# Optimization experiments

Measured on AMD Instinct MI355X. Metric: run time of the kernel, lower is better.

## Reference

```python
import jax, jax.numpy as jnp
import numpy as np

N = 50000      # nodes
E = 800000     # edges (avg degree 16)
D = 64         # emb_dim
L = 5          # num_layer
BN_EPS = 1e-5


def setup_inputs() -> dict:
    key = jax.random.key(0)
    ks = jax.random.split(key, 10)
    x = jax.random.randint(ks[0], (N,), 0, 1)                      # indices into 1-row embedding
    edge_index = jax.random.randint(ks[1], (2, E), 0, N)
    edge_attr = jax.random.normal(ks[2], (E, 7), dtype=jnp.float32)
    s = lambda k, shape: (jax.random.normal(k, shape, dtype=jnp.float32) * 0.05)
    node_emb = s(ks[3], (1, D))
    # per-layer GINConv params, stacked on a leading layer axis for lax.scan
    We = s(ks[4], (L, 7, D));   be = jnp.zeros((L, D), jnp.float32)      # edge_encoder
    eps = jnp.zeros((L,), jnp.float32)                                   # GIN eps
    W1 = s(ks[5], (L, D, 2 * D)); b1 = jnp.zeros((L, 2 * D), jnp.float32)  # mlp linear1
    g1 = jnp.ones((L, 2 * D), jnp.float32); bb1 = jnp.zeros((L, 2 * D), jnp.float32)  # mlp BN
    W2 = s(ks[6], (L, 2 * D, D)); b2 = jnp.zeros((L, D), jnp.float32)    # mlp linear2
    g2 = jnp.ones((L, D), jnp.float32); bb2 = jnp.zeros((L, D), jnp.float32)  # outer BN
    return dict(x=x, edge_index=edge_index, edge_attr=edge_attr, node_emb=node_emb,
                We=We, be=be, eps=eps, W1=W1, b1=b1, g1=g1, bb1=bb1,
                W2=W2, b2=b2, g2=g2, bb2=bb2)


def _bn(a, g, b):
    # BatchNorm1d in training mode: batch statistics over node axis, biased var
    m = a.mean(axis=0)
    v = jnp.var(a, axis=0)
    return (a - m) * jax.lax.rsqrt(v + BN_EPS) * g + b


def reference(x, edge_index, edge_attr, node_emb, We, be, eps,
              W1, b1, g1, bb1, W2, b2, g2, bb2):
    src, dst = edge_index[0], edge_index[1]
    h = node_emb[x]                                    # [N, D]
    relu_flags = jnp.arange(L) < (L - 1)               # ReLU on all but last layer

    def step(h, p):
        We_, be_, eps_, W1_, b1_, g1_, bb1_, W2_, b2_, g2_, bb2_, flag = p
        ee = edge_attr @ We_ + be_                     # [E, D] edge embeddings
        msg = jax.nn.relu(h[src] + ee)                 # gather + elementwise
        agg = jax.ops.segment_sum(msg, dst, num_segments=N)  # scatter-add
        z = (1.0 + eps_) * h + agg                     # GIN combine
        a = jax.nn.relu(_bn(z @ W1_ + b1_, g1_, bb1_)) # mlp: lin -> BN -> ReLU
        hb = _bn(a @ W2_ + b2_, g2_, bb2_)             # lin -> outer BN
        h_new = jnp.where(flag, jax.nn.relu(hb), hb)   # dropout omitted (eval)
        return h_new, None

    h, _ = jax.lax.scan(step, h, (We, be, eps, W1, b1, g1, bb1, W2, b2, g2, bb2, relu_flags))
    return h                                           # JK='last'
```

## Files before the change

kernel.cpp:

```cpp
#include <hip/hip_runtime.h>
#include <hip/hip_fp16.h>

#define NN 50000
#define EE 800000
#define NB 782
#define NBKT 196
#define CAP8 736

typedef _Float16 f16x8 __attribute__((ext_vector_type(8)));
typedef _Float16 f16x4 __attribute__((ext_vector_type(4)));
typedef _Float16 f16x2 __attribute__((ext_vector_type(2)));
typedef float f32x4 __attribute__((ext_vector_type(4)));

__device__ __forceinline__ unsigned h2u(__half2 h) {
    union { __half2 h; unsigned u; } c; c.h = h; return c.u;
}
__device__ __forceinline__ f16x2 u2h(unsigned u) {
    union { unsigned u; f16x2 h; } c; c.u = u; return c.h;
}

__global__ __launch_bounds__(256) void bin_kernel(
    const int* __restrict__ ei, const float* __restrict__ ea,
    int* __restrict__ bktcur, int4* __restrict__ srec,
    unsigned short* __restrict__ sdst)
{
    __shared__ int cnt[NBKT], base[NBKT];
    const int t = threadIdx.x;
    const int xid = blockIdx.x & 7;
    if (t < NBKT) cnt[t] = 0;
    __syncthreads();
    const int e0 = blockIdx.x << 10;
    int bkk[4], rk[4], loc[4];
#pragma unroll
    for (int j = 0; j < 4; ++j) {
        const int e = e0 + (j << 8) + t;
        if (e < EE) {
            const int d = ei[EE + e];
            bkk[j] = d >> 8;
            loc[j] = d & 255;
            rk[j] = atomicAdd(&cnt[bkk[j]], 1);
        } else bkk[j] = -1;
    }
    __syncthreads();
    if (t < NBKT) base[t] = cnt[t] ? atomicAdd(&bktcur[(t << 3) + xid], cnt[t]) : 0;
    __syncthreads();
#pragma unroll
    for (int j = 0; j < 4; ++j) {
        if (bkk[j] < 0) continue;
        const int slot = base[bkk[j]] + rk[j];
        if (slot >= CAP8) continue;
        const int pos = ((bkk[j] << 3) + xid) * CAP8 + slot;
        const int e = e0 + (j << 8) + t;
        const int src = ei[e];
        const float* a = ea + e * 7;
        const unsigned h0 = __half_as_ushort(__float2half(a[0]));
        const unsigned h1 = __half_as_ushort(__float2half(a[1]));
        const unsigned h2 = __half_as_ushort(__float2half(a[2]));
        const unsigned h3 = __half_as_ushort(__float2half(a[3]));
        const unsigned h4 = __half_as_ushort(__float2half(a[4]));
        const unsigned h5 = __half_as_ushort(__float2half(a[5]));
        const unsigned h6 = __half_as_ushort(__float2half(a[6]));
        srec[pos] = make_int4((int)(h0 | (h1 << 16)), (int)(h2 | (h3 << 16)),
                              (int)(h4 | (h5 << 16)), (int)(h6 | ((unsigned)src << 16)));
        sdst[pos] = (unsigned short)loc[j];
    }
}

__global__ __launch_bounds__(256) void bcountA_kernel(
    const int* __restrict__ bktcur, const unsigned short* __restrict__ sdst,
    int* __restrict__ deg, int* __restrict__ bsum)
{
    __shared__ int nc[256], sm[256];
    const int b = blockIdx.x, t = threadIdx.x;
    nc[t] = 0;
    __syncthreads();
    for (int x = 0; x < 8; ++x) {
        const int nE = min(bktcur[(b << 3) + x], CAP8);
        const int sb = ((b << 3) + x) * CAP8;
        for (int i = t; i < nE; i += 256) atomicAdd(&nc[(int)sdst[sb + i]], 1);
    }
    __syncthreads();
    const int node = (b << 8) + t;
    if (node < NN) deg[node] = nc[t];
    sm[t] = (node < NN) ? ((nc[t] + 7) & ~7) : 0;
    __syncthreads();
    for (int o = 128; o > 0; o >>= 1) {
        if (t < o) sm[t] += sm[t + o];
        __syncthreads();
    }
    if (t == 0) bsum[b] = sm[0];
}

__global__ __launch_bounds__(256) void scanB_kernel(int* __restrict__ bsum) {
    __shared__ int sm[256];
    const int t = threadIdx.x;
    const int v = (t < 196) ? bsum[t] : 0;
    sm[t] = v;
    __syncthreads();
    for (int o = 1; o < 256; o <<= 1) {
        const int u = (t >= o) ? sm[t - o] : 0;
        __syncthreads();
        sm[t] += u;
        __syncthreads();
    }
    bsum[t] = sm[t] - v;
}

__global__ __launch_bounds__(256) void scanC_kernel(const int* __restrict__ deg,
                                                    const int* __restrict__ bsum,
                                                    int* __restrict__ off) {
    __shared__ int sm[256];
    const int t = threadIdx.x;
    const int i = (blockIdx.x << 8) + t;
    const int v = (i < NN) ? ((deg[i] + 7) & ~7) : 0;
    sm[t] = v;
    __syncthreads();
    for (int o = 1; o < 256; o <<= 1) {
        const int u = (t >= o) ? sm[t - o] : 0;
        __syncthreads();
        sm[t] += u;
        __syncthreads();
    }
    const int excl = bsum[blockIdx.x] + sm[t] - v;
    if (i < NN) off[i] = excl;
    else if (i == NN) off[NN] = excl;
}

__global__ __launch_bounds__(256) void place2_kernel(
    const int* __restrict__ bktcur, const int* __restrict__ off,
    const int4* __restrict__ srec, const unsigned short* __restrict__ sdst,
    int4* __restrict__ pea)
{
    __shared__ int curs[256];
    const int b = blockIdx.x, t = threadIdx.x;
    const int node = (b << 8) + t;
    curs[t] = (node < NN) ? off[node] : 0;
    __syncthreads();
    for (int x = 0; x < 8; ++x) {
        const int nE = min(bktcur[(b << 3) + x], CAP8);
        const int sb = ((b << 3) + x) * CAP8;
        for (int i = t; i < nE; i += 256) {
            const int ln = (int)sdst[sb + i];
            const int p = atomicAdd(&curs[ln], 1);
            pea[p] = srec[sb + i];
        }
    }
    __syncthreads();
    if (node < NN) {
        const int end = off[node + 1];
        for (int p = curs[t]; p < end; ++p)
            pea[p] = make_int4(0, 0, 0, (int)(((unsigned)NN) << 16));
    }
}

__global__ __launch_bounds__(256) void bnstats_kernel(
    const float* __restrict__ part, const int nb, const int half,
    const float* __restrict__ g, const float* __restrict__ bb,
    float* __restrict__ scsh)
{
    __shared__ float ss[256], qq[256];
    const int c = blockIdx.x, t = threadIdx.x;
    const int stride = half << 1;
    float s = 0.f, q = 0.f;
    for (int b = t; b < nb; b += 256) {
        s += part[b * stride + c];
        q += part[b * stride + half + c];
    }
    ss[t] = s; qq[t] = q;
    __syncthreads();
    for (int o = 128; o > 0; o >>= 1) {
        if (t < o) { ss[t] += ss[t + o]; qq[t] += qq[t + o]; }
        __syncthreads();
    }
    if (t == 0) {
        const float m = ss[0] * (1.0f / NN);
        const float v = fmaxf(qq[0] * (1.0f / NN) - m * m, 0.0f);
        const float sc = g[c] * rsqrtf(v + 1e-5f);
        scsh[c] = sc;
        scsh[half + c] = bb[c] - m * sc;
    }
}

__global__ __launch_bounds__(256) void wprep_kernel(
    const float* __restrict__ W1, const float* __restrict__ W2,
    const float* __restrict__ We, const float* __restrict__ be,
    _Float16* __restrict__ W1s, _Float16* __restrict__ W2s,
    unsigned* __restrict__ Wepk, unsigned* __restrict__ be2)
{
    const int i = (blockIdx.x << 8) + threadIdx.x;
    if (i < 40960) {
        const int l = i >> 13, j = i & 8191, k = j >> 7, n = j & 127;
        W1s[(l << 13) + ((((k >> 3) << 7) + n) << 3) + (k & 7)] = (_Float16)W1[i];
    } else if (i < 81920) {
        const int i2 = i - 40960;
        const int l = i2 >> 13, j = i2 & 8191, k = j >> 6, n = j & 63;
        W2s[(l << 13) + ((((k >> 3) << 6) + n) << 3) + (k & 7)] = (_Float16)W2[i2];
    } else if (i < 83040) {
        const int i3 = i - 81920;
        const int l = i3 / 224;
        const int r = i3 - l * 224;
        const int k = r >> 5, s = r & 31;
        const float* W = We + l * 448 + (k << 6) + (s << 1);
        Wepk[i3] = h2u(__floats2half2_rn(W[0], W[1]));
    } else if (i < 83200) {
        const int i4 = i - 83040;
        const int l = i4 >> 5, s = i4 & 31;
        const float* B = be + (l << 6) + (s << 1);
        be2[i4] = h2u(__floats2half2_rn(B[0], B[1]));
    }
}

__global__ __launch_bounds__(256) void hprep_kernel(
    const float* __restrict__ y2, const float* __restrict__ scsh2,
    __half* __restrict__ h16)
{
    const int i4 = (blockIdx.x << 8) + threadIdx.x;
    const float4 v = ((const float4*)y2)[i4];
    const int d0 = (i4 << 2) & 63;
    const float a = fmaxf(fmaf(v.x, scsh2[d0 + 0], scsh2[64 + d0 + 0]), 0.f);
    const float b = fmaxf(fmaf(v.y, scsh2[d0 + 1], scsh2[64 + d0 + 1]), 0.f);
    const float c = fmaxf(fmaf(v.z, scsh2[d0 + 2], scsh2[64 + d0 + 2]), 0.f);
    const float d = fmaxf(fmaf(v.w, scsh2[d0 + 3], scsh2[64 + d0 + 3]), 0.f);
    *(int2*)(h16 + (i4 << 2)) =
        make_int2((int)h2u(__floats2half2_rn(a, b)),
                  (int)h2u(__floats2half2_rn(c, d)));
}

__global__ __launch_bounds__(256) void hprep0_kernel(
    const int* __restrict__ x, const float* __restrict__ nemb,
    __half* __restrict__ h16, unsigned* __restrict__ z32)
{
    const int i4 = (blockIdx.x << 8) + threadIdx.x;
    if (blockIdx.x == 0 && threadIdx.x < 32)
        ((unsigned*)h16)[(NN << 5) + threadIdx.x] = 0xFBFFFBFFu;
    if (i4 < 1536) z32[1600000 + i4] = 0u;
    const int n = i4 >> 4;
    const float4 v = ((const float4*)nemb)[(x[n] << 4) + (i4 & 15)];
    *(int2*)(h16 + (i4 << 2)) =
        make_int2((int)h2u(__floats2half2_rn(v.x, v.y)),
                  (int)h2u(__floats2half2_rn(v.z, v.w)));
}

__global__ __launch_bounds__(256) void gather_kernel(
    const int* __restrict__ off, const int4* __restrict__ pea,
    const unsigned* __restrict__ h32,
    const unsigned* __restrict__ Wepk, const unsigned* __restrict__ be2,
    const float* __restrict__ epsp,
    unsigned* __restrict__ z32)
{
    const int t = threadIdx.x;
    const int lane = t & 63;
    const int s = lane & 31;
    const int n = (blockIdx.x << 3) + ((t >> 6) << 1) + (lane >> 5);

    const f16x2 w0 = u2h(Wepk[s]),       w1 = u2h(Wepk[32 + s]),
                w2 = u2h(Wepk[64 + s]),  w3 = u2h(Wepk[96 + s]),
                w4 = u2h(Wepk[128 + s]), w5 = u2h(Wepk[160 + s]),
                w6 = u2h(Wepk[192 + s]);
    const f16x2 beh = u2h(be2[s]);

    const int e0 = off[n], e1 = off[n + 1];

    f16x2 acc2 = (f16x2){(_Float16)0.f, (_Float16)0.f};
    for (int e = e0; e < e1; e += 8) {
        int4 pk[8];
#pragma unroll
        for (int j = 0; j < 8; ++j) pk[j] = pea[e + j];
        unsigned hv[8];
#pragma unroll
        for (int j = 0; j < 8; ++j) {
            const int src = (int)(((unsigned)pk[j].w) >> 16);
            hv[j] = h32[(src << 5) + s];
        }
#pragma unroll
        for (int j = 0; j < 8; ++j) {
            const f16x2 a01 = u2h((unsigned)pk[j].x);
            const f16x2 a23 = u2h((unsigned)pk[j].y);
            const f16x2 a45 = u2h((unsigned)pk[j].z);
            const f16x2 a6x = u2h((unsigned)pk[j].w);
            f16x2 ee = beh;
            ee += (f16x2){a01[0], a01[0]} * w0;
            ee += (f16x2){a01[1], a01[1]} * w1;
            ee += (f16x2){a23[0], a23[0]} * w2;
            ee += (f16x2){a23[1], a23[1]} * w3;
            ee += (f16x2){a45[0], a45[0]} * w4;
            ee += (f16x2){a45[1], a45[1]} * w5;
            ee += (f16x2){a6x[0], a6x[0]} * w6;
            f16x2 m2 = u2h(hv[j]) + ee;
            const _Float16 zz = (_Float16)0.f;
            m2 = (f16x2){ m2[0] > zz ? m2[0] : zz, m2[1] > zz ? m2[1] : zz };
            acc2 += m2;
        }
    }
    const f16x2 hn2 = u2h(h32[(n << 5) + s]);
    const float e1f = 1.0f + epsp[0];
    const float zLo = fmaf(e1f, (float)hn2[0], (float)acc2[0]);
    const float zHi = fmaf(e1f, (float)hn2[1], (float)acc2[1]);
    z32[(n << 5) + s] = h2u(__floats2half2_rn(zLo, zHi));
}

__global__ __launch_bounds__(256) void mm1_kernel(
    const _Float16* __restrict__ z16, const _Float16* __restrict__ W1s,
    const float* __restrict__ b1p, _Float16* __restrict__ y1h,
    float* __restrict__ part1)
{
    __shared__ float smS[4][128], smQ[4][128];
    const int t = threadIdx.x;
    const int wv = t >> 6, lane = t & 63;
    const int q = lane >> 4, ln = lane & 15;
    const int r0 = blockIdx.x << 6;

    const int rowm = r0 + (wv << 4) + ln;
    const f16x8 af0 = *(const f16x8*)(z16 + rowm * 64 + (q << 3));
    const f16x8 af1 = *(const f16x8*)(z16 + rowm * 64 + 32 + (q << 3));

    f32x4 acc[8];
#pragma unroll
    for (int n0 = 0; n0 < 8; ++n0) acc[n0] = (f32x4){0.f, 0.f, 0.f, 0.f};
#pragma unroll
    for (int n0 = 0; n0 < 8; ++n0) {
        const f16x8 bf0 = *(const f16x8*)(W1s + (((q << 7) + (n0 << 4) + ln) << 3));
        const f16x8 bf1 = *(const f16x8*)(W1s + ((((4 + q) << 7) + (n0 << 4) + ln) << 3));
        acc[n0] = __builtin_amdgcn_mfma_f32_16x16x32_f16(af0, bf0, acc[n0], 0, 0, 0);
        acc[n0] = __builtin_amdgcn_mfma_f32_16x16x32_f16(af1, bf1, acc[n0], 0, 0, 0);
    }

    const int baseRow = r0 + (wv << 4) + (q << 2);
#pragma unroll
    for (int n0 = 0; n0 < 8; ++n0) {
        const int col = (n0 << 4) + ln;
        const float bb = b1p[col];
        float s = 0.f, sq = 0.f;
#pragma unroll
        for (int rg = 0; rg < 4; ++rg) {
            const int row = baseRow + rg;
            const float y = acc[n0][rg] + bb;
            y1h[row * 128 + col] = (_Float16)y;
            const float m = (row < NN) ? 1.f : 0.f;
            s = fmaf(m, y, s); sq = fmaf(m, y * y, sq);
        }
        s += __shfl_xor(s, 16); s += __shfl_xor(s, 32);
        sq += __shfl_xor(sq, 16); sq += __shfl_xor(sq, 32);
        if (lane < 16) { smS[wv][col] = s; smQ[wv][col] = sq; }
    }
    __syncthreads();
    if (t < 128) {
        const float s = smS[0][t] + smS[1][t] + smS[2][t] + smS[3][t];
        const float q2 = smQ[0][t] + smQ[1][t] + smQ[2][t] + smQ[3][t];
        part1[(blockIdx.x << 8) + t] = s;
        part1[(blockIdx.x << 8) + 128 + t] = q2;
    }
}

__global__ __launch_bounds__(256) void mm2_kernel(
    const _Float16* __restrict__ y1h, const float* __restrict__ scsh1,
    const _Float16* __restrict__ W2s, const float* __restrict__ b2,
    float* __restrict__ y2, float* __restrict__ part2)
{
    __shared__ float smS[4][64], smQ[4][64];
    const int t = threadIdx.x;
    const int wv = t >> 6, lane = t & 63;
    const int q = lane >> 4, ln = lane & 15;
    const int r0 = blockIdx.x << 6;

    const int rowm = r0 + (wv << 4) + ln;
    f16x8 af[4];
#pragma unroll
    for (int ks = 0; ks < 4; ++ks) {
        const int k0 = (ks << 5) + (q << 3);
        const f16x8 raw = *(const f16x8*)(y1h + rowm * 128 + k0);
        const float4 scA = *(const float4*)(scsh1 + k0);
        const float4 scB = *(const float4*)(scsh1 + k0 + 4);
        const float4 shA = *(const float4*)(scsh1 + 128 + k0);
        const float4 shB = *(const float4*)(scsh1 + 128 + k0 + 4);
        const float sc[8] = {scA.x, scA.y, scA.z, scA.w, scB.x, scB.y, scB.z, scB.w};
        const float sh[8] = {shA.x, shA.y, shA.z, shA.w, shB.x, shB.y, shB.z, shB.w};
        f16x8 a;
#pragma unroll
        for (int j = 0; j < 8; ++j)
            a[j] = (_Float16)fmaxf(fmaf((float)raw[j], sc[j], sh[j]), 0.f);
        af[ks] = a;
    }

    f32x4 acc[4];
#pragma unroll
    for (int n0 = 0; n0 < 4; ++n0) acc[n0] = (f32x4){0.f, 0.f, 0.f, 0.f};
#pragma unroll
    for (int n0 = 0; n0 < 4; ++n0) {
#pragma unroll
        for (int ks = 0; ks < 4; ++ks) {
            const f16x8 bf = *(const f16x8*)(
                W2s + (((((ks << 2) + q) << 6) + (n0 << 4) + ln) << 3));
            acc[n0] = __builtin_amdgcn_mfma_f32_16x16x32_f16(af[ks], bf, acc[n0], 0, 0, 0);
        }
    }

    const int baseRow = r0 + (wv << 4) + (q << 2);
#pragma unroll
    for (int n0 = 0; n0 < 4; ++n0) {
        const int col = (n0 << 4) + ln;
        const float bb = b2[col];
        float s = 0.f, sq = 0.f;
#pragma unroll
        for (int rg = 0; rg < 4; ++rg) {
            const int row = baseRow + rg;
            const float y = acc[n0][rg] + bb;
            y2[row * 64 + col] = y;
            const float m = (row < NN) ? 1.f : 0.f;
            s = fmaf(m, y, s); sq = fmaf(m, y * y, sq);
        }
        s += __shfl_xor(s, 16); s += __shfl_xor(s, 32);
        sq += __shfl_xor(sq, 16); sq += __shfl_xor(sq, 32);
        if (lane < 16) { smS[wv][col] = s; smQ[wv][col] = sq; }
    }
    __syncthreads();
    if (t < 64) {
        const float s = smS[0][t] + smS[1][t] + smS[2][t] + smS[3][t];
        const float q2 = smQ[0][t] + smQ[1][t] + smQ[2][t] + smQ[3][t];
        part2[(blockIdx.x << 7) + t] = s;
        part2[(blockIdx.x << 7) + 64 + t] = q2;
    }
}

__global__ __launch_bounds__(256) void final_kernel(
    const float* __restrict__ y2, const float* __restrict__ scsh2,
    float* __restrict__ out)
{
    const int i = (blockIdx.x << 8) + threadIdx.x;
    if (i >= NN * 64) return;
    const int d = i & 63;
    out[i] = fmaf(y2[i], scsh2[d], scsh2[64 + d]);
}

extern "C" void kernel_launch(void* const* d_in, const int* in_sizes, int n_in,
                              void* d_out, int out_size, void* d_ws, size_t ws_size,
                              hipStream_t stream)
{
    const int*   x    = (const int*)d_in[0];
    const int*   ei   = (const int*)d_in[1];
    const float* ea   = (const float*)d_in[2];
    const float* nemb = (const float*)d_in[3];
    const float* We   = (const float*)d_in[4];
    const float* be   = (const float*)d_in[5];
    const float* eps  = (const float*)d_in[6];
    const float* W1   = (const float*)d_in[7];
    const float* b1   = (const float*)d_in[8];
    const float* g1   = (const float*)d_in[9];
    const float* bb1  = (const float*)d_in[10];
    const float* W2   = (const float*)d_in[11];
    const float* b2   = (const float*)d_in[12];
    const float* g2   = (const float*)d_in[13];
    const float* bb2  = (const float*)d_in[14];
    float* out = (float*)d_out;

    int*      iws   = (int*)d_ws;
    float*    fws   = (float*)d_ws;
    int*      off   = iws + 0;
    int*      deg   = iws + 50048;
    int*      bsum  = iws + 150144;
    float*    scsh1 = fws + 150400;
    float*    scsh2 = fws + 150656;
    float*    part1 = fws + 150784;
    float*    part2 = fws + 350976;
    _Float16* W1s   = (_Float16*)(fws + 451072);
    _Float16* W2s   = (_Float16*)(fws + 471552);
    unsigned* Wepk  = (unsigned*)(fws + 492032);
    unsigned* be2   = (unsigned*)(fws + 493152);
    int4*     pea   = (int4*)(iws + 493312);
    _Float16* z16   = (_Float16*)(fws + 5093312);
    _Float16* y1h   = (_Float16*)(fws + 6694848);
    float*    y2    = fws + 6694848;
    __half*   h16   = (__half*)(fws + 9897920);

    int4*           srec   = (int4*)(fws + 5093312);
    unsigned short* sdst   = (unsigned short*)(fws + 9897920);
    int*            bktcur = iws + 150784;

    hipMemsetAsync(bktcur, 0, NBKT * 8 * sizeof(int), stream);

    bin_kernel    <<<782,  256, 0, stream>>>(ei, ea, bktcur, srec, sdst);
    bcountA_kernel<<<NBKT, 256, 0, stream>>>(bktcur, sdst, deg, bsum);
    scanB_kernel  <<<1,    256, 0, stream>>>(bsum);
    scanC_kernel  <<<196,  256, 0, stream>>>(deg, bsum, off);
    place2_kernel <<<NBKT, 256, 0, stream>>>(bktcur, off, srec, sdst, pea);
    wprep_kernel  <<<325,  256, 0, stream>>>(W1, W2, We, be, W1s, W2s, Wepk, be2);
    hprep0_kernel <<<3125, 256, 0, stream>>>(x, nemb, h16, (unsigned*)z16);

    for (int l = 0; l < 5; ++l) {
        gather_kernel<<<6250, 256, 0, stream>>>(
            off, pea, (const unsigned*)h16, Wepk + l * 224, be2 + l * 32,
            eps + l, (unsigned*)z16);

        mm1_kernel<<<NB, 256, 0, stream>>>(z16, W1s + l * 8192, b1 + l * 128,
                                           y1h, part1);

        bnstats_kernel<<<128, 256, 0, stream>>>(part1, NB, 128,
                                                g1 + l * 128, bb1 + l * 128, scsh1);

        mm2_kernel<<<NB, 256, 0, stream>>>(y1h, scsh1, W2s + l * 8192, b2 + l * 64,
                                           y2, part2);

        bnstats_kernel<<<64, 256, 0, stream>>>(part2, NB, 64,
                                               g2 + l * 64, bb2 + l * 64, scsh2);

        if (l < 4)
            hprep_kernel<<<3125, 256, 0, stream>>>(y2, scsh2, h16);
    }

    final_kernel<<<12500, 256, 0, stream>>>(y2, scsh2, out);
}
```

Before: 454.6 us.

## Fuse BN stats into matmul kernels via last-block reduction; coarsen edge binning

Removes the two separate bnstats launches per layer. mm1 and mm2 now accumulate per-channel sum and sum-of-squares into 8 striped global atomic buffers, and the last block to finish, detected with an atomic counter, computes the BN scale and shift. Separately, the binning pass drops the 8-way sub-bucket split, uses one bucket per 256 destination nodes with a larger capacity, and processes 4096 edges per block. This saves ten kernel launches and the partial-sum round trip, in exchange for global float atomics, a threadfence and higher contention on the bucket cursors.

Result: slower. 652.6 us (+43.6%).

```diff
diff --git a/kernel.cpp b/kernel.cpp
--- a/kernel.cpp
+++ b/kernel.cpp
@@ -5,10 +5,9 @@
 #define EE 800000
 #define NB 782
 #define NBKT 196
-#define CAP8 736
+#define BCAP 4608
 
 typedef _Float16 f16x8 __attribute__((ext_vector_type(8)));
-typedef _Float16 f16x4 __attribute__((ext_vector_type(4)));
 typedef _Float16 f16x2 __attribute__((ext_vector_type(2)));
 typedef float f32x4 __attribute__((ext_vector_type(4)));
 
@@ -26,30 +25,30 @@
 {
     __shared__ int cnt[NBKT], base[NBKT];
     const int t = threadIdx.x;
-    const int xid = blockIdx.x & 7;
     if (t < NBKT) cnt[t] = 0;
     __syncthreads();
-    const int e0 = blockIdx.x << 10;
-    int bkk[4], rk[4], loc[4];
-#pragma unroll
-    for (int j = 0; j < 4; ++j) {
+    const int e0 = blockIdx.x << 12;
+    int meta[16];
+#pragma unroll
+    for (int j = 0; j < 16; ++j) {
         const int e = e0 + (j << 8) + t;
         if (e < EE) {
             const int d = ei[EE + e];
-            bkk[j] = d >> 8;
-            loc[j] = d & 255;
-            rk[j] = atomicAdd(&cnt[bkk[j]], 1);
-        } else bkk[j] = -1;
-    }
-    __syncthreads();
-    if (t < NBKT) base[t] = cnt[t] ? atomicAdd(&bktcur[(t << 3) + xid], cnt[t]) : 0;
-    __syncthreads();
-#pragma unroll
-    for (int j = 0; j < 4; ++j) {
-        if (bkk[j] < 0) continue;
-        const int slot = base[bkk[j]] + rk[j];
-        if (slot >= CAP8) continue;
-        const int pos = ((bkk[j] << 3) + xid) * CAP8 + slot;
+            const int bk = d >> 8;
+            const int rk = atomicAdd(&cnt[bk], 1);
+            meta[j] = (rk << 16) | (bk << 8) | (d & 255);
+        } else meta[j] = -1;
+    }
+    __syncthreads();
+    if (t < NBKT) base[t] = cnt[t] ? atomicAdd(&bktcur[t], cnt[t]) : 0;
+    __syncthreads();
+#pragma unroll
+    for (int j = 0; j < 16; ++j) {
+        if (meta[j] < 0) continue;
+        const int bk = (meta[j] >> 8) & 255;
+        const int slot = base[bk] + (meta[j] >> 16);
+        if (slot >= BCAP) continue;
+        const int pos = bk * BCAP + slot;
         const int e = e0 + (j << 8) + t;
         const int src = ei[e];
         const float* a = ea + e * 7;
@@ -62,7 +61,7 @@
         const unsigned h6 = __half_as_ushort(__float2half(a[6]));
         srec[pos] = make_int4((int)(h0 | (h1 << 16)), (int)(h2 | (h3 << 16)),
                               (int)(h4 | (h5 << 16)), (int)(h6 | ((unsigned)src << 16)));
-        sdst[pos] = (unsigned short)loc[j];
+        sdst[pos] = (unsigned short)(meta[j] & 255);
     }
 }
 
@@ -74,11 +73,9 @@
     const int b = blockIdx.x, t = threadIdx.x;
     nc[t] = 0;
     __syncthreads();
-    for (int x = 0; x < 8; ++x) {
-        const int nE = min(bktcur[(b << 3) + x], CAP8);
-        const int sb = ((b << 3) + x) * CAP8;
-        for (int i = t; i < nE; i += 256) atomicAdd(&nc[(int)sdst[sb + i]], 1);
-    }
+    const int nE = min(bktcur[b], BCAP);
+    const int sb = b * BCAP;
+    for (int i = t; i < nE; i += 256) atomicAdd(&nc[(int)sdst[sb + i]], 1);
     __syncthreads();
     const int node = (b << 8) + t;
     if (node < NN) deg[node] = nc[t];
@@ -136,48 +133,18 @@
     const int node = (b << 8) + t;
     curs[t] = (node < NN) ? off[node] : 0;
     __syncthreads();
-    for (int x = 0; x < 8; ++x) {
-        const int nE = min(bktcur[(b << 3) + x], CAP8);
-        const int sb = ((b << 3) + x) * CAP8;
-        for (int i = t; i < nE; i += 256) {
-            const int ln = (int)sdst[sb + i];
-            const int p = atomicAdd(&curs[ln], 1);
-            pea[p] = srec[sb + i];
-        }
+    const int nE = min(bktcur[b], BCAP);
+    const int sb = b * BCAP;
+    for (int i = t; i < nE; i += 256) {
+        const int ln = (int)sdst[sb + i];
+        const int p = atomicAdd(&curs[ln], 1);
+        pea[p] = srec[sb + i];
     }
     __syncthreads();
     if (node < NN) {
         const int end = off[node + 1];
         for (int p = curs[t]; p < end; ++p)
             pea[p] = make_int4(0, 0, 0, (int)(((unsigned)NN) << 16));
-    }
-}
-
-__global__ __launch_bounds__(256) void bnstats_kernel(
-    const float* __restrict__ part, const int nb, const int half,
-    const float* __restrict__ g, const float* __restrict__ bb,
-    float* __restrict__ scsh)
-{
-    __shared__ float ss[256], qq[256];
-    const int c = blockIdx.x, t = threadIdx.x;
-    const int stride = half << 1;
-    float s = 0.f, q = 0.f;
-    for (int b = t; b < nb; b += 256) {
-        s += part[b * stride + c];
-        q += part[b * stride + half + c];
-    }
-    ss[t] = s; qq[t] = q;
-    __syncthreads();
-    for (int o = 128; o > 0; o >>= 1) {
-        if (t < o) { ss[t] += ss[t + o]; qq[t] += qq[t + o]; }
-        __syncthreads();
-    }
-    if (t == 0) {
-        const float m = ss[0] * (1.0f / NN);
-        const float v = fmaxf(qq[0] * (1.0f / NN) - m * m, 0.0f);
-        const float sc = g[c] * rsqrtf(v + 1e-5f);
-        scsh[c] = sc;
-        scsh[half + c] = bb[c] - m * sc;
     }
 }
 
@@ -302,9 +269,12 @@
 __global__ __launch_bounds__(256) void mm1_kernel(
     const _Float16* __restrict__ z16, const _Float16* __restrict__ W1s,
     const float* __restrict__ b1p, _Float16* __restrict__ y1h,
-    float* __restrict__ part1)
+    float* __restrict__ accL, int* __restrict__ cntp,
+    const float* __restrict__ g1p, const float* __restrict__ bb1p,
+    float* __restrict__ scsh1)
 {
     __shared__ float smS[4][128], smQ[4][128];
+    __shared__ int lastFlag;
     const int t = threadIdx.x;
     const int wv = t >> 6, lane = t & 63;
     const int q = lane >> 4, ln = lane & 15;
@@ -345,19 +315,43 @@
     }
     __syncthreads();
     if (t < 128) {
-        const float s = smS[0][t] + smS[1][t] + smS[2][t] + smS[3][t];
-        const float q2 = smQ[0][t] + smQ[1][t] + smQ[2][t] + smQ[3][t];
-        part1[(blockIdx.x << 8) + t] = s;
-        part1[(blockIdx.x << 8) + 128 + t] = q2;
+        const float s4 = smS[0][t] + smS[1][t] + smS[2][t] + smS[3][t];
+        const float q4 = smQ[0][t] + smQ[1][t] + smQ[2][t] + smQ[3][t];
+        float* a1 = accL + ((blockIdx.x & 7) * 384);
+        atomicAdd(&a1[t], s4);
+        atomicAdd(&a1[128 + t], q4);
+    }
+    __syncthreads();
+    if (t == 0) {
+        __threadfence();
+        lastFlag = (atomicAdd(cntp, 1) == NB - 1) ? 1 : 0;
+    }
+    __syncthreads();
+    if (lastFlag && t < 128) {
+        float ss = 0.f, qq2 = 0.f;
+#pragma unroll
+        for (int c = 0; c < 8; ++c) {
+            ss  += atomicAdd(accL + c * 384 + t, 0.0f);
+            qq2 += atomicAdd(accL + c * 384 + 128 + t, 0.0f);
+        }
+        const float m = ss * (1.0f / NN);
+        const float v = fmaxf(qq2 * (1.0f / NN) - m * m, 0.0f);
+        const float sc = g1p[t] * rsqrtf(v + 1e-5f);
+        scsh1[t] = sc;
+        scsh1[128 + t] = bb1p[t] - m * sc;
     }
 }
 
 __global__ __launch_bounds__(256) void mm2_kernel(
     const _Float16* __restrict__ y1h, const float* __restrict__ scsh1,
     const _Float16* __restrict__ W2s, const float* __restrict__ b2,
-    float* __restrict__ y2, float* __restrict__ part2)
+    float* __restrict__ y2,
+    float* __restrict__ accL, int* __restrict__ cntp,
+    const float* __restrict__ g2p, const float* __restrict__ bb2p,
+    float* __restrict__ scsh2)
 {
     __shared__ float smS[4][64], smQ[4][64];
+    __shared__ int lastFlag;
     const int t = threadIdx.x;
     const int wv = t >> 6, lane = t & 63;
     const int q = lane >> 4, ln = lane & 15;
@@ -415,10 +409,30 @@
     }
     __syncthreads();
     if (t < 64) {
-        const float s = smS[0][t] + smS[1][t] + smS[2][t] + smS[3][t];
-        const float q2 = smQ[0][t] + smQ[1][t] + smQ[2][t] + smQ[3][t];
-        part2[(blockIdx.x << 7) + t] = s;
-        part2[(blockIdx.x << 7) + 64 + t] = q2;
+        const float s4 = smS[0][t] + smS[1][t] + smS[2][t] + smS[3][t];
+        const float q4 = smQ[0][t] + smQ[1][t] + smQ[2][t] + smQ[3][t];
+        float* a2p = accL + ((blockIdx.x & 7) * 384) + 256;
+        atomicAdd(&a2p[t], s4);
+        atomicAdd(&a2p[64 + t], q4);
+    }
+    __syncthreads();
+    if (t == 0) {
+        __threadfence();
+        lastFlag = (atomicAdd(cntp, 1) == NB - 1) ? 1 : 0;
+    }
+    __syncthreads();
+    if (lastFlag && t < 64) {
+        float ss = 0.f, qq2 = 0.f;
+#pragma unroll
+        for (int c = 0; c < 8; ++c) {
+            ss  += atomicAdd(accL + c * 384 + 256 + t, 0.0f);
+            qq2 += atomicAdd(accL + c * 384 + 320 + t, 0.0f);
+        }
+        const float m = ss * (1.0f / NN);
+        const float v = fmaxf(qq2 * (1.0f / NN) - m * m, 0.0f);
+        const float sc = g2p[t] * rsqrtf(v + 1e-5f);
+        scsh2[t] = sc;
+        scsh2[64 + t] = bb2p[t] - m * sc;
     }
 }
 
@@ -460,8 +474,9 @@
     int*      bsum  = iws + 150144;
     float*    scsh1 = fws + 150400;
     float*    scsh2 = fws + 150656;
-    float*    part1 = fws + 150784;
-    float*    part2 = fws + 350976;
+    int*      bktcur= iws + 150784;
+    int*      cntrs = iws + 150980;
+    float*    accbuf= fws + 151040;
     _Float16* W1s   = (_Float16*)(fws + 451072);
     _Float16* W2s   = (_Float16*)(fws + 471552);
     unsigned* Wepk  = (unsigned*)(fws + 492032);
@@ -472,13 +487,12 @@
     float*    y2    = fws + 6694848;
     __half*   h16   = (__half*)(fws + 9897920);
 
-    int4*           srec   = (int4*)(fws + 5093312);
-    unsigned short* sdst   = (unsigned short*)(fws + 9897920);
-    int*            bktcur = iws + 150784;
-
-    hipMemsetAsync(bktcur, 0, NBKT * 8 * sizeof(int), stream);
-
-    bin_kernel    <<<782,  256, 0, stream>>>(ei, ea, bktcur, srec, sdst);
+    int4*           srec = (int4*)(fws + 5093312);
+    unsigned short* sdst = (unsigned short*)(fws + 9897920);
+
+    hipMemsetAsync(bktcur, 0, (166400 - 150784) * sizeof(int), stream);
+
+    bin_kernel    <<<196,  256, 0, stream>>>(ei, ea, bktcur, srec, sdst);
     bcountA_kernel<<<NBKT, 256, 0, stream>>>(bktcur, sdst, deg, bsum);
     scanB_kernel  <<<1,    256, 0, stream>>>(bsum);
     scanC_kernel  <<<196,  256, 0, stream>>>(deg, bsum, off);
@@ -491,17 +505,13 @@
             off, pea, (const unsigned*)h16, Wepk + l * 224, be2 + l * 32,
             eps + l, (unsigned*)z16);
 
-        mm1_kernel<<<NB, 256, 0, stream>>>(z16, W1s + l * 8192, b1 + l * 128,
-                                           y1h, part1);
-
-        bnstats_kernel<<<128, 256, 0, stream>>>(part1, NB, 128,
-                                                g1 + l * 128, bb1 + l * 128, scsh1);
-
-        mm2_kernel<<<NB, 256, 0, stream>>>(y1h, scsh1, W2s + l * 8192, b2 + l * 64,
-                                           y2, part2);
-
-        bnstats_kernel<<<64, 256, 0, stream>>>(part2, NB, 64,
-                                               g2 + l * 64, bb2 + l * 64, scsh2);
+        mm1_kernel<<<NB, 256, 0, stream>>>(
+            z16, W1s + l * 8192, b1 + l * 128, y1h,
+            accbuf + l * 3072, cntrs + l, g1 + l * 128, bb1 + l * 128, scsh1);
+
+        mm2_kernel<<<NB, 256, 0, stream>>>(
+            y1h, scsh1, W2s + l * 8192, b2 + l * 64, y2,
+            accbuf + l * 3072, cntrs + 5 + l, g2 + l * 64, bb2 + l * 64, scsh2);
 
         if (l < 4)
             hprep_kernel<<<3125, 256, 0, stream>>>(y2, scsh2, h16);
```
